# Kernel tuning notes

Hardware: AMD Instinct MI355X
Metric: run time of the kernel (lower is better)

Reference implementation:

```python
import jax, jax.numpy as jnp
import numpy as np

DIM = 64  # per-head dim used for the sqrt scale


def setup_inputs() -> dict:
    key = jax.random.key(0)
    kq, kk, kv, ke, kf = jax.random.split(key, 5)
    B, N, d, k = 32, 4096, 64, 256
    Q = jax.random.normal(kq, (B, N, d), dtype=jnp.float32)
    K = jax.random.normal(kk, (B, N, d), dtype=jnp.float32)
    V = jax.random.normal(kv, (B, N, d), dtype=jnp.float32)
    E = jax.random.normal(ke, (N, k), dtype=jnp.float32) * (1.0 / np.sqrt(N))
    F = jax.random.normal(kf, (N, k), dtype=jnp.float32) * (1.0 / np.sqrt(N))
    return {"Q": Q, "K": K, "V": V, "E": E, "F": F}


def reference(Q, K, V, E, F):
    # Linformer head: K^T E -> [B,d,k]; Q (K^T E) / sqrt(d) -> [B,N,k]
    K_proj = jnp.einsum('bnd,nk->bdk', K, E)          # low-rank key projection
    scores = jnp.einsum('bnd,bdk->bnk', Q, K_proj) / jnp.sqrt(jnp.float32(DIM))
    P_bar = jax.nn.softmax(scores, axis=2)            # [B,N,k]
    # (V^T F)^T -> [B,k,d]
    V_proj = jnp.einsum('bnd,nk->bkd', V, F)
    return jnp.einsum('bnk,bkd->bnd', P_bar, V_proj)  # [B,N,d]
```

## Files before the change

kernel.cpp:

```cpp
#include <hip/hip_runtime.h>
#include <hip/hip_bf16.h>

#define BB 32
#define NN 4096
#define DDIM 64

typedef __attribute__((ext_vector_type(8)))  short bf16x8;
typedef __attribute__((ext_vector_type(16))) float f32x16;
typedef __attribute__((ext_vector_type(4)))  float f32x4;

static __device__ inline unsigned short f2bf(float x) {
  union { float f; unsigned u; } v; v.f = x;
  unsigned r = (v.u + 0x7FFFu + ((v.u >> 16) & 1u)) >> 16;
  return (unsigned short)r;
}

static __device__ inline unsigned pk(float a, float b) {
  union { __hip_bfloat162 h; unsigned u; } c;
  c.h = __float22bfloat162_rn(float2{a, b});
  return c.u;
}

static __device__ inline bf16x8 pack8(const float* f) {
  union { unsigned u[4]; bf16x8 v; } r;
  r.u[0] = pk(f[0], f[1]); r.u[1] = pk(f[2], f[3]);
  r.u[2] = pk(f[4], f[5]); r.u[3] = pk(f[6], f[7]);
  return r.v;
}

template <int SA, int SB>
static __device__ inline void load_set(
    const float* __restrict__ pA, const float* __restrict__ pB, int t,
    float a0[8], float a1[8], float b0[8], float b1[8])
{
  const float* qA = pA + (long)t * 16 * SA;
  const float* qB = pB + (long)t * 16 * SB;
#pragma unroll
  for (int j = 0; j < 8; ++j) {
    a0[j] = qA[j * SA];      a1[j] = qA[j * SA + 32];
    b0[j] = qB[j * SB];      b1[j] = qB[j * SB + 32];
  }
}

static __device__ inline void mfma4(
    f32x16 acc[2][2],
    const float a0[8], const float a1[8], const float b0[8], const float b1[8])
{
  bf16x8 A0 = pack8(a0), A1 = pack8(a1);
  bf16x8 B0 = pack8(b0), B1 = pack8(b1);
  acc[0][0] = __builtin_amdgcn_mfma_f32_32x32x16_bf16(A0, B0, acc[0][0], 0, 0, 0);
  acc[0][1] = __builtin_amdgcn_mfma_f32_32x32x16_bf16(A0, B1, acc[0][1], 0, 0, 0);
  acc[1][0] = __builtin_amdgcn_mfma_f32_32x32x16_bf16(A1, B0, acc[1][0], 0, 0, 0);
  acc[1][1] = __builtin_amdgcn_mfma_f32_32x32x16_bf16(A1, B1, acc[1][1], 0, 0, 0);
}

template <int SA, int SB, int OS, int NCH>
static __device__ inline void proj_body(
    const float* __restrict__ As, const float* __restrict__ Bs,
    float* __restrict__ Cg, int mAdd, int nAdd, int chunk, int h, int lr)
{
  constexpr int CN = NN / NCH;
  constexpr int T  = CN / 16;

  f32x16 acc[2][2];
#pragma unroll
  for (int i = 0; i < 2; ++i)
#pragma unroll
    for (int j = 0; j < 2; ++j)
#pragma unroll
      for (int q = 0; q < 16; ++q) acc[i][j][q] = 0.f;

  const int n0 = chunk * CN + h * 8;
  const float* pA = As + (long)n0 * SA + mAdd + lr;
  const float* pB = Bs + (long)n0 * SB + nAdd + lr;

  float xa0[8], xa1[8], xb0[8], xb1[8];
  float ya0[8], ya1[8], yb0[8], yb1[8];

  load_set<SA, SB>(pA, pB, 0, xa0, xa1, xb0, xb1);

  for (int tt = 0; tt < T; tt += 2) {
    load_set<SA, SB>(pA, pB, tt + 1, ya0, ya1, yb0, yb1);
    mfma4(acc, xa0, xa1, xb0, xb1);
    const int tn = (tt + 2 < T) ? (tt + 2) : 0;
    load_set<SA, SB>(pA, pB, tn, xa0, xa1, xb0, xb1);
    mfma4(acc, ya0, ya1, yb0, yb1);
  }

#pragma unroll
  for (int mt = 0; mt < 2; ++mt)
#pragma unroll
    for (int nt = 0; nt < 2; ++nt)
#pragma unroll
      for (int i = 0; i < 16; ++i) {
        int ro  = (i & 3) + 8 * (i >> 2) + 4 * h;
        int row = mAdd + mt * 32 + ro;
        int col = nAdd + nt * 32 + lr;
        Cg[row * OS + col] = acc[mt][nt][i];
      }
}

template <int NCH>
__global__ __launch_bounds__(256, 2) void proj_gemm(
    const float* __restrict__ Kg, const float* __restrict__ Vg,
    const float* __restrict__ Eg, const float* __restrict__ Fg,
    float* __restrict__ KpP, float* __restrict__ VpP)
{
  const int blk = blockIdx.x;
  const int chunk = blk % NCH;
  const int mat = (blk / NCH) & 1, b = blk / (2 * NCH);
  const int t = threadIdx.x, w = t >> 6, l = t & 63, h = l >> 5, lr = l & 31;
  const long PSTR = (long)BB * 16384;

  if (mat == 0) {
    proj_body<256, 64, 64, NCH>(Eg, Kg + (long)b * NN * DDIM,
                                KpP + (long)chunk * PSTR + b * 16384,
                                w * 64, 0, chunk, h, lr);
  } else {
    proj_body<64, 256, 256, NCH>(Vg + (long)b * NN * DDIM, Fg,
                                 VpP + (long)chunk * PSTR + b * 16384,
                                 0, w * 64, chunk, h, lr);
  }
}

template <int NCH>
__global__ __launch_bounds__(256) void reduce_cvt(
    const float* __restrict__ KpP, const float* __restrict__ VpP,
    unsigned short* __restrict__ Kpb, unsigned short* __restrict__ Vpb)
{
  const int blk = blockIdx.x;
  const float* src = (blk < 256) ? KpP : VpP;
  unsigned short* dst = (blk < 256) ? Kpb : Vpb;
  const long i = (long)(blk & 255) * 2048 + threadIdx.x * 8;
  float a[8];
#pragma unroll
  for (int j = 0; j < 8; ++j) a[j] = 0.f;
#pragma unroll
  for (int cch = 0; cch < NCH; ++cch) {
    const float4 p0 = *(const float4*)(src + (long)cch * (BB * 16384) + i);
    const float4 p1 = *(const float4*)(src + (long)cch * (BB * 16384) + i + 4);
    a[0] += p0.x; a[1] += p0.y; a[2] += p0.z; a[3] += p0.w;
    a[4] += p1.x; a[5] += p1.y; a[6] += p1.z; a[7] += p1.w;
  }
  unsigned short o[8];
#pragma unroll
  for (int j = 0; j < 8; ++j) o[j] = f2bf(a[j]);
  *(bf16x8*)(dst + i) = *(const bf16x8*)&o[0];
}

__global__ __launch_bounds__(256, 2) void attn2_kernel(
    const float* __restrict__ Qg, const unsigned short* __restrict__ Kpb,
    const unsigned short* __restrict__ Vpb, float* __restrict__ Og)
{
  extern __shared__ float O_lds[];

  const int blk = blockIdx.x;
  const int b = blk >> 4, rg = blk & 15;
  const int t = threadIdx.x, w = t >> 6, l = t & 63;
  const int h = l >> 5, lr = l & 31;
  const int rbase = rg * 256 + w * 64;

  const unsigned short* Kp = Kpb + (long)b * 16384;
  const unsigned short* Vp = Vpb + (long)b * 16384;

  bf16x8 Bq[2][4];
#pragma unroll
  for (int rt = 0; rt < 2; ++rt)
#pragma unroll
    for (int kk = 0; kk < 4; ++kk) {
      const float* qp = Qg + ((long)b * NN + rbase + rt * 32 + lr) * 64 + kk * 16 + h * 8;
      float4 x = *(const float4*)qp;
      float4 y = *(const float4*)(qp + 4);
      union { unsigned u[4]; bf16x8 v; } r;
      r.u[0] = pk(x.x, x.y); r.u[1] = pk(x.z, x.w);
      r.u[2] = pk(y.x, y.y); r.u[3] = pk(y.z, y.w);
      Bq[rt][kk] = r.v;
    }

  f32x16 o[2][2];
#pragma unroll
  for (int rt = 0; rt < 2; ++rt)
#pragma unroll
    for (int dt = 0; dt < 2; ++dt)
#pragma unroll
      for (int q = 0; q < 16; ++q) o[rt][dt][q] = 0.f;
  float rowpart[2] = {0.f, 0.f};

  union UV { uint4 u; bf16x8 v; };

#pragma unroll
  for (int kt = 0; kt < 8; ++kt) {
    bf16x8 Ak[4];
#pragma unroll
    for (int kk = 0; kk < 4; ++kk)
      Ak[kk] = *(const bf16x8*)(Kp + (long)(kt * 32 + lr) * 64 + kk * 16 + h * 8);
    bf16x8 Av[2][2];
#pragma unroll
    for (int dt = 0; dt < 2; ++dt)
#pragma unroll
      for (int kc = 0; kc < 2; ++kc)
        Av[dt][kc] = *(const bf16x8*)(Vp + (long)(dt * 32 + lr) * 256 + (kt * 2 + kc) * 16 + h * 8);

#pragma unroll
    for (int rt = 0; rt < 2; ++rt) {
      f32x16 s;
#pragma unroll
      for (int q = 0; q < 16; ++q) s[q] = 0.f;
#pragma unroll
      for (int kk = 0; kk < 4; ++kk)
        s = __builtin_amdgcn_mfma_f32_32x32x16_bf16(Ak[kk], Bq[rt][kk], s, 0, 0, 0);

      float p[16];
#pragma unroll
      for (int q = 0; q < 16; ++q) p[q] = exp2f(s[q] * 0.1803368801f);
      rowpart[rt] += (((p[0] + p[1]) + (p[2] + p[3])) + ((p[4] + p[5]) + (p[6] + p[7])))
                   + (((p[8] + p[9]) + (p[10] + p[11])) + ((p[12] + p[13]) + (p[14] + p[15])));

      unsigned wv[8];
#pragma unroll
      for (int m = 0; m < 8; ++m) wv[m] = pk(p[2 * m], p[2 * m + 1]);
      unsigned r02 = __shfl_xor(h ? wv[0] : wv[2], 32);
      unsigned r13 = __shfl_xor(h ? wv[1] : wv[3], 32);
      unsigned r46 = __shfl_xor(h ? wv[4] : wv[6], 32);
      unsigned r57 = __shfl_xor(h ? wv[5] : wv[7], 32);
      UV c0, c1;
      if (h == 0) {
        c0.u = uint4{wv[0], wv[1], r02, r13};
        c1.u = uint4{wv[4], wv[5], r46, r57};
      } else {
        c0.u = uint4{r02, r13, wv[2], wv[3]};
        c1.u = uint4{r46, r57, wv[6], wv[7]};
      }
      o[rt][0] = __builtin_amdgcn_mfma_f32_32x32x16_bf16(Av[0][0], c0.v, o[rt][0], 0, 0, 0);
      o[rt][0] = __builtin_amdgcn_mfma_f32_32x32x16_bf16(Av[0][1], c1.v, o[rt][0], 0, 0, 0);
      o[rt][1] = __builtin_amdgcn_mfma_f32_32x32x16_bf16(Av[1][0], c0.v, o[rt][1], 0, 0, 0);
      o[rt][1] = __builtin_amdgcn_mfma_f32_32x32x16_bf16(Av[1][1], c1.v, o[rt][1], 0, 0, 0);
    }
  }

#pragma unroll
  for (int rt = 0; rt < 2; ++rt) {
    float rowsum = rowpart[rt] + __shfl_xor(rowpart[rt], 32);
    float inv = __builtin_amdgcn_rcpf(rowsum);
    const int r = w * 64 + rt * 32 + lr;
#pragma unroll
    for (int dt = 0; dt < 2; ++dt)
#pragma unroll
      for (int qg = 0; qg < 4; ++qg) {
        f32x4 vq;
        vq[0] = o[rt][dt][qg * 4 + 0] * inv;
        vq[1] = o[rt][dt][qg * 4 + 1] * inv;
        vq[2] = o[rt][dt][qg * 4 + 2] * inv;
        vq[3] = o[rt][dt][qg * 4 + 3] * inv;
        int cd = dt * 8 + 2 * qg + h;
        int cp = cd ^ (r & 15);
        *(f32x4*)&O_lds[r * 64 + cp * 4] = vq;
      }
  }
  __syncthreads();

  const long obase = ((long)b * NN + rg * 256) * 64;
#pragma unroll
  for (int i = 0; i < 16; ++i) {
    int ci = i * 256 + t;
    int rr = ci >> 4, cc = ci & 15, cp = cc ^ (rr & 15);
    *(float4*)(Og + obase + rr * 64 + cc * 4) = *(const float4*)&O_lds[rr * 64 + cp * 4];
  }
}

extern "C" void kernel_launch(void* const* d_in, const int* in_sizes, int n_in,
                              void* d_out, int out_size, void* d_ws, size_t ws_size,
                              hipStream_t stream) {
  const float* Q = (const float*)d_in[0];
  const float* K = (const float*)d_in[1];
  const float* V = (const float*)d_in[2];
  const float* E = (const float*)d_in[3];
  const float* F = (const float*)d_in[4];
  float* out = (float*)d_out;

  char* ws = (char*)d_ws;
  const long SLAB = (long)BB * 16384 * 4;

  hipFuncSetAttribute((const void*)attn2_kernel,
                      hipFuncAttributeMaxDynamicSharedMemorySize, 65536);

  if (ws_size >= (size_t)(16 * SLAB + (2l << 20))) {
    float*          KpP = (float*)(ws);
    float*          VpP = (float*)(ws + 8 * SLAB);
    unsigned short* Kpb = (unsigned short*)(ws + 16 * SLAB);
    unsigned short* Vpb = Kpb + 524288;

    proj_gemm<8><<<dim3(512), dim3(256), 0, stream>>>(K, V, E, F, KpP, VpP);
    reduce_cvt<8><<<dim3(512), dim3(256), 0, stream>>>(KpP, VpP, Kpb, Vpb);
    attn2_kernel<<<dim3(512), dim3(256), 65536, stream>>>(Q, Kpb, Vpb, out);
  } else {
    float*          KpP = (float*)(ws);
    float*          VpP = (float*)(ws + 4 * SLAB);
    unsigned short* Kpb = (unsigned short*)(ws + 8 * SLAB);
    unsigned short* Vpb = Kpb + 524288;

    proj_gemm<4><<<dim3(256), dim3(256), 0, stream>>>(K, V, E, F, KpP, VpP);
    reduce_cvt<4><<<dim3(512), dim3(256), 0, stream>>>(KpP, VpP, Kpb, Vpb);
    attn2_kernel<<<dim3(512), dim3(256), 65536, stream>>>(Q, Kpb, Vpb, out);
  }
}
```

Measured before the change: 190.8 us.

## Stage projection GEMM operands through double-buffered LDS with coalesced loads

Measured after the change: 185.0 us. 1.03x faster.

```diff
diff --git a/kernel.cpp b/kernel.cpp
--- a/kernel.cpp
+++ b/kernel.cpp
@@ -21,46 +21,20 @@
   return c.u;
 }
 
-static __device__ inline bf16x8 pack8(const float* f) {
-  union { unsigned u[4]; bf16x8 v; } r;
-  r.u[0] = pk(f[0], f[1]); r.u[1] = pk(f[2], f[3]);
-  r.u[2] = pk(f[4], f[5]); r.u[3] = pk(f[6], f[7]);
-  return r.v;
-}
-
-template <int SA, int SB>
-static __device__ inline void load_set(
-    const float* __restrict__ pA, const float* __restrict__ pB, int t,
-    float a0[8], float a1[8], float b0[8], float b1[8])
-{
-  const float* qA = pA + (long)t * 16 * SA;
-  const float* qB = pB + (long)t * 16 * SB;
-#pragma unroll
-  for (int j = 0; j < 8; ++j) {
-    a0[j] = qA[j * SA];      a1[j] = qA[j * SA + 32];
-    b0[j] = qB[j * SB];      b1[j] = qB[j * SB + 32];
-  }
-}
-
-static __device__ inline void mfma4(
-    f32x16 acc[2][2],
-    const float a0[8], const float a1[8], const float b0[8], const float b1[8])
-{
-  bf16x8 A0 = pack8(a0), A1 = pack8(a1);
-  bf16x8 B0 = pack8(b0), B1 = pack8(b1);
-  acc[0][0] = __builtin_amdgcn_mfma_f32_32x32x16_bf16(A0, B0, acc[0][0], 0, 0, 0);
-  acc[0][1] = __builtin_amdgcn_mfma_f32_32x32x16_bf16(A0, B1, acc[0][1], 0, 0, 0);
-  acc[1][0] = __builtin_amdgcn_mfma_f32_32x32x16_bf16(A1, B0, acc[1][0], 0, 0, 0);
-  acc[1][1] = __builtin_amdgcn_mfma_f32_32x32x16_bf16(A1, B1, acc[1][1], 0, 0, 0);
-}
-
-template <int SA, int SB, int OS, int NCH>
-static __device__ inline void proj_body(
-    const float* __restrict__ As, const float* __restrict__ Bs,
-    float* __restrict__ Cg, int mAdd, int nAdd, int chunk, int h, int lr)
+template <int MAT, int NCH>
+static __device__ inline void proj_core(
+    const float* __restrict__ Gbig,
+    const float* __restrict__ Gsml,
+    float* __restrict__ Cg,
+    unsigned short (*lds)[10240],
+    int t, int w, int l, int h, int lr, int chunk)
 {
   constexpr int CN = NN / NCH;
-  constexpr int T  = CN / 16;
+  constexpr int T  = CN / 32;
+
+  const int n00 = chunk * CN;
+  const float* pb = Gbig + (long)n00 * 256 + t;
+  const float* ps = Gsml + (long)(n00 + w * 8) * 64 + l;
 
   f32x16 acc[2][2];
 #pragma unroll
@@ -70,23 +44,75 @@
 #pragma unroll
       for (int q = 0; q < 16; ++q) acc[i][j][q] = 0.f;
 
-  const int n0 = chunk * CN + h * 8;
-  const float* pA = As + (long)n0 * SA + mAdd + lr;
-  const float* pB = Bs + (long)n0 * SB + nAdd + lr;
-
-  float xa0[8], xa1[8], xb0[8], xb1[8];
-  float ya0[8], ya1[8], yb0[8], yb1[8];
-
-  load_set<SA, SB>(pA, pB, 0, xa0, xa1, xb0, xb1);
-
+  float xb[32], xs[8], yb[32], ys[8];
+
+  auto loadset = [&](float (&vb)[32], float (&vs)[8], int step) {
+    const float* qb = pb + (long)step * (32 * 256);
+    const float* qs = ps + (long)step * (32 * 64);
+#pragma unroll
+    for (int i = 0; i < 32; ++i) vb[i] = qb[(long)i * 256];
+#pragma unroll
+    for (int i = 0; i < 8; ++i)  vs[i] = qs[(long)i * 64];
+  };
+
+  auto writeset = [&](int buf, float (&vb)[32], float (&vs)[8]) {
+#pragma unroll
+    for (int g = 0; g < 4; ++g) {
+      union { unsigned u[4]; bf16x8 v; } r;
+      r.u[0] = pk(vb[g * 8 + 0], vb[g * 8 + 1]);
+      r.u[1] = pk(vb[g * 8 + 2], vb[g * 8 + 3]);
+      r.u[2] = pk(vb[g * 8 + 4], vb[g * 8 + 5]);
+      r.u[3] = pk(vb[g * 8 + 6], vb[g * 8 + 7]);
+      *(bf16x8*)&lds[buf][(g * 256 + t) * 8] = r.v;
+    }
+    {
+      union { unsigned u[4]; bf16x8 v; } r;
+      r.u[0] = pk(vs[0], vs[1]); r.u[1] = pk(vs[2], vs[3]);
+      r.u[2] = pk(vs[4], vs[5]); r.u[3] = pk(vs[6], vs[7]);
+      *(bf16x8*)&lds[buf][8192 + (w * 64 + l) * 8] = r.v;
+    }
+  };
+
+  auto consume = [&](int buf) {
+#pragma unroll
+    for (int s2 = 0; s2 < 2; ++s2) {
+      const int g = s2 * 2 + h;
+      bf16x8 B0 = *(const bf16x8*)&lds[buf][(g * 256 + w * 64 + lr) * 8];
+      bf16x8 B1 = *(const bf16x8*)&lds[buf][(g * 256 + w * 64 + 32 + lr) * 8];
+      bf16x8 S0 = *(const bf16x8*)&lds[buf][8192 + (g * 64 + lr) * 8];
+      bf16x8 S1 = *(const bf16x8*)&lds[buf][8192 + (g * 64 + 32 + lr) * 8];
+      if (MAT == 0) {
+        acc[0][0] = __builtin_amdgcn_mfma_f32_32x32x16_bf16(B0, S0, acc[0][0], 0, 0, 0);
+        acc[0][1] = __builtin_amdgcn_mfma_f32_32x32x16_bf16(B0, S1, acc[0][1], 0, 0, 0);
+        acc[1][0] = __builtin_amdgcn_mfma_f32_32x32x16_bf16(B1, S0, acc[1][0], 0, 0, 0);
+        acc[1][1] = __builtin_amdgcn_mfma_f32_32x32x16_bf16(B1, S1, acc[1][1], 0, 0, 0);
+      } else {
+        acc[0][0] = __builtin_amdgcn_mfma_f32_32x32x16_bf16(S0, B0, acc[0][0], 0, 0, 0);
+        acc[0][1] = __builtin_amdgcn_mfma_f32_32x32x16_bf16(S0, B1, acc[0][1], 0, 0, 0);
+        acc[1][0] = __builtin_amdgcn_mfma_f32_32x32x16_bf16(S1, B0, acc[1][0], 0, 0, 0);
+        acc[1][1] = __builtin_amdgcn_mfma_f32_32x32x16_bf16(S1, B1, acc[1][1], 0, 0, 0);
+      }
+    }
+  };
+
+  loadset(xb, xs, 0);
+  loadset(yb, ys, 1);
+
+#pragma unroll 1
   for (int tt = 0; tt < T; tt += 2) {
-    load_set<SA, SB>(pA, pB, tt + 1, ya0, ya1, yb0, yb1);
-    mfma4(acc, xa0, xa1, xb0, xb1);
-    const int tn = (tt + 2 < T) ? (tt + 2) : 0;
-    load_set<SA, SB>(pA, pB, tn, xa0, xa1, xb0, xb1);
-    mfma4(acc, ya0, ya1, yb0, yb1);
-  }
-
+    writeset(0, xb, xs);
+    if (tt + 2 < T) loadset(xb, xs, tt + 2);
+    __syncthreads();
+    consume(0);
+    writeset(1, yb, ys);
+    if (tt + 3 < T) loadset(yb, ys, tt + 3);
+    __syncthreads();
+    consume(1);
+  }
+
+  const int mAdd = (MAT == 0) ? w * 64 : 0;
+  const int nAdd = (MAT == 0) ? 0 : w * 64;
+  const int OS   = (MAT == 0) ? 64 : 256;
 #pragma unroll
   for (int mt = 0; mt < 2; ++mt)
 #pragma unroll
@@ -106,6 +132,8 @@
     const float* __restrict__ Eg, const float* __restrict__ Fg,
     float* __restrict__ KpP, float* __restrict__ VpP)
 {
+  __shared__ unsigned short lds[2][10240];
+
   const int blk = blockIdx.x;
   const int chunk = blk % NCH;
   const int mat = (blk / NCH) & 1, b = blk / (2 * NCH);
@@ -113,13 +141,11 @@
   const long PSTR = (long)BB * 16384;
 
   if (mat == 0) {
-    proj_body<256, 64, 64, NCH>(Eg, Kg + (long)b * NN * DDIM,
-                                KpP + (long)chunk * PSTR + b * 16384,
-                                w * 64, 0, chunk, h, lr);
+    proj_core<0, NCH>(Eg, Kg + (long)b * NN * DDIM,
+                      KpP + (long)chunk * PSTR + b * 16384, lds, t, w, l, h, lr, chunk);
   } else {
-    proj_body<64, 256, 256, NCH>(Vg + (long)b * NN * DDIM, Fg,
-                                 VpP + (long)chunk * PSTR + b * 16384,
-                                 0, w * 64, chunk, h, lr);
+    proj_core<1, NCH>(Fg, Vg + (long)b * NN * DDIM,
+                      VpP + (long)chunk * PSTR + b * 16384, lds, t, w, l, h, lr, chunk);
   }
 }
 
```
